# Optimization experiments

Measured on AMD Instinct MI355X. Metric: run time of the kernel, lower is better.

Reference implementation:

```python
import jax, jax.numpy as jnp
import numpy as np
import math

NUM_HEADS = 8
LN_EPS = 1e-8


def setup_inputs() -> dict:
    key = jax.random.key(0)
    ks = jax.random.split(key, 8)
    B, S, D = 16, 1024, 1024
    s = 1.0 / math.sqrt(D)
    return {
        "queries": jax.random.normal(ks[0], (B, S, D), dtype=jnp.float32),
        "keys": jax.random.normal(ks[1], (B, S, D), dtype=jnp.float32),
        "Wq": jax.random.normal(ks[2], (D, D), dtype=jnp.float32) * s,
        "bq": jnp.zeros((D,), dtype=jnp.float32),
        "Wk": jax.random.normal(ks[3], (D, D), dtype=jnp.float32) * s,
        "bk": jnp.zeros((D,), dtype=jnp.float32),
        "Wv": jax.random.normal(ks[4], (D, D), dtype=jnp.float32) * s,
        "bv": jnp.zeros((D,), dtype=jnp.float32),
        "ln_gamma": jnp.ones((D,), dtype=jnp.float32),
        "ln_beta": jnp.zeros((D,), dtype=jnp.float32),
    }


def _split_heads(x, H):
    # [B, S, D] -> [B*H, S, D/H], batch-major flattening (b*H + h), matching torch
    B, S, D = x.shape
    d = D // H
    return x.reshape(B, S, H, d).transpose(0, 2, 1, 3).reshape(B * H, S, d)


def _merge_heads(x, B, H):
    # [B*H, S, d] -> [B, S, H*d]
    BH, S, d = x.shape
    return x.reshape(B, H, S, d).transpose(0, 2, 1, 3).reshape(B, S, H * d)


def reference(queries, keys, Wq, bq, Wk, bk, Wv, bv, ln_gamma, ln_beta):
    B, S, D = queries.shape
    K_len = keys.shape[1]
    H = NUM_HEADS

    # ReLU'd QKV projections (nn.Linear uses x @ W.T + b)
    Q = jax.nn.relu(jnp.einsum("bsd,ed->bse", queries, Wq) + bq)
    K = jax.nn.relu(jnp.einsum("bsd,ed->bse", keys, Wk) + bk)
    V = jax.nn.relu(jnp.einsum("bsd,ed->bse", keys, Wv) + bv)

    Q_ = _split_heads(Q, H)  # [B*H, S, d]
    K_ = _split_heads(K, H)
    V_ = _split_heads(V, H)
    d_k = K_.shape[-1]

    scores = jnp.einsum("nsd,ntd->nst", Q_, K_) / jnp.sqrt(jnp.float32(d_k))
    attn = jax.nn.softmax(scores, axis=-1)  # [B*H, S, K_len]

    # post-softmax multiplicative mask: mask of nonzero query rows, tiled
    # head-major (mask.repeat(H,1,1)) exactly as the torch code does
    mask = (jnp.sum(jnp.abs(queries), axis=-1, keepdims=True) > 0).astype(queries.dtype)  # [B, S, 1]
    mask = jnp.broadcast_to(mask, (B, S, K_len))
    mask = jnp.tile(mask, (H, 1, 1))  # [H*B, S, K_len], index i -> batch i % B
    attn = attn * mask
    # dropout is identity in eval mode

    out = jnp.einsum("nst,ntd->nsd", attn, V_)  # [B*H, S, d]
    out = _merge_heads(out, B, H)  # [B, S, D]
    out = out + queries

    # LayerNorm over last dim, eps=1e-8
    mu = jnp.mean(out, axis=-1, keepdims=True)
    var = jnp.mean(jnp.square(out - mu), axis=-1, keepdims=True)
    out = (out - mu) / jnp.sqrt(var + LN_EPS) * ln_gamma + ln_beta
    return out
```

## Files before the change

kernel.cpp:

```cpp
#include <hip/hip_runtime.h>
#include <hip/hip_bf16.h>

#define B_ 16
#define S_ 1024
#define D_ 1024
#define H_ 8

typedef __attribute__((ext_vector_type(4))) float f32x4;
typedef __attribute__((ext_vector_type(8))) short s16x8;
typedef __attribute__((ext_vector_type(4))) short s16x4;
typedef unsigned int u32;

static __device__ __forceinline__ short f2bf(float x) {
  union { __hip_bfloat16 h; short s; } cv;
  cv.h = __float2bfloat16(x);
  return cv.s;
}
static __device__ __forceinline__ float bf2f(short x) {
  union { float f; u32 u; } cv;
  cv.u = ((u32)(unsigned short)x) << 16;
  return cv.f;
}
static __device__ __forceinline__ void async16(const void* g, void* l) {
  __builtin_amdgcn_global_load_lds((const __attribute__((address_space(1))) u32*)g,
                                   (__attribute__((address_space(3))) u32*)l, 16, 0, 0);
}

__global__ __launch_bounds__(256) void cvt_bf16(const float* __restrict__ s,
                                                short* __restrict__ d, int n8) {
  int i = blockIdx.x * 256 + threadIdx.x;
  if (i >= n8) return;
  const float4* s4 = (const float4*)s;
  float4 a = s4[2 * i], b = s4[2 * i + 1];
  s16x8 r;
  r[0] = f2bf(a.x); r[1] = f2bf(a.y); r[2] = f2bf(a.z); r[3] = f2bf(a.w);
  r[4] = f2bf(b.x); r[5] = f2bf(b.y); r[6] = f2bf(b.z); r[7] = f2bf(b.w);
  *(s16x8*)(d + (size_t)i * 8) = r;
}

__global__ __launch_bounds__(256, 2) void gemm_qkv(
    const short* __restrict__ qb, const short* __restrict__ kb,
    const short* __restrict__ wq, const short* __restrict__ wk,
    const short* __restrict__ wv, const float* __restrict__ bq,
    const float* __restrict__ bk, const float* __restrict__ bv,
    short* __restrict__ Qb, short* __restrict__ Kb, short* __restrict__ Vb) {
  __shared__ short lA[128 * 64];
  __shared__ short lB[128 * 64];
  const short* A; const short* W; const float* bias; short* C;
  switch (blockIdx.z) {
    case 0:  A = qb; W = wq; bias = bq; C = Qb; break;
    case 1:  A = kb; W = wk; bias = bk; C = Kb; break;
    default: A = kb; W = wv; bias = bv; C = Vb; break;
  }
  const int t = threadIdx.x;
  const int w = t >> 6, l = t & 63, lg = l >> 4, li = l & 15;
  const int wr = w >> 1, wc = w & 1;
  const int m0 = blockIdx.y << 7, n0 = blockIdx.x << 7;

  f32x4 acc[4][4];
#pragma unroll
  for (int m = 0; m < 4; ++m)
#pragma unroll
    for (int n = 0; n < 4; ++n) acc[m][n] = {0.f, 0.f, 0.f, 0.f};

  const char* Ab = (const char*)A + (size_t)m0 * 2048;
  const char* Wb = (const char*)W + (size_t)n0 * 2048;

#pragma unroll 1
  for (int k0 = 0; k0 < 1024; k0 += 64) {
    __syncthreads();
#pragma unroll
    for (int it = 0; it < 4; ++it) {
      int e = it * 256 + t;
      int row = e >> 3;
      int sb = ((e & 7) << 4) ^ ((row & 7) << 4);
      async16(Ab + (size_t)row * 2048 + k0 * 2 + sb, (char*)lA + e * 16);
      async16(Wb + (size_t)row * 2048 + k0 * 2 + sb, (char*)lB + e * 16);
    }
    __syncthreads();
#pragma unroll
    for (int kk = 0; kk < 2; ++kk) {
      s16x8 af[4], bfr[4];
#pragma unroll
      for (int m = 0; m < 4; ++m) {
        int row = wr * 64 + m * 16 + li;
        af[m] = *(const s16x8*)((char*)lA + row * 128 +
                                ((kk * 64 + (lg << 4)) ^ ((row & 7) << 4)));
      }
#pragma unroll
      for (int n = 0; n < 4; ++n) {
        int row = wc * 64 + n * 16 + li;
        bfr[n] = *(const s16x8*)((char*)lB + row * 128 +
                                 ((kk * 64 + (lg << 4)) ^ ((row & 7) << 4)));
      }
#pragma unroll
      for (int m = 0; m < 4; ++m)
#pragma unroll
        for (int n = 0; n < 4; ++n)
          acc[m][n] = __builtin_amdgcn_mfma_f32_16x16x32_bf16(af[m], bfr[n],
                                                              acc[m][n], 0, 0, 0);
    }
  }
#pragma unroll
  for (int n = 0; n < 4; ++n) {
    int col = n0 + wc * 64 + n * 16 + li;
    float bb = bias[col];
#pragma unroll
    for (int m = 0; m < 4; ++m) {
      int row0 = m0 + wr * 64 + m * 16 + (lg << 2);
#pragma unroll
      for (int r = 0; r < 4; ++r) {
        float v = acc[m][n][r] + bb;
        C[(size_t)(row0 + r) * 1024 + col] = f2bf(v > 0.f ? v : 0.f);
      }
    }
  }
}

__global__ __launch_bounds__(256, 2) void attn_kernel(
    const short* __restrict__ Qb, const short* __restrict__ Kb,
    const short* __restrict__ Vb, short* __restrict__ Ob) {
  __shared__ short lK[64 * 128];
  __shared__ short lV[128 * 72];
  __shared__ short lP[128 * 64];

  const int t = threadIdx.x;
  const int w = t >> 6, l = t & 63, lg = l >> 4, li = l & 15;
  const int bh = blockIdx.y;
  const int b = bh >> 3, h = bh & 7;
  const int q0 = blockIdx.x << 7;
  const size_t hbase = (size_t)b * (S_ * D_) + h * 128;

  s16x8 qf[2][4];
#pragma unroll
  for (int m = 0; m < 2; ++m)
#pragma unroll
    for (int kk = 0; kk < 4; ++kk) {
      int row = q0 + (w << 5) + m * 16 + li;
      qf[m][kk] = *(const s16x8*)(Qb + hbase + (size_t)row * D_ + kk * 32 + (lg << 3));
    }

  f32x4 o[2][8];
#pragma unroll
  for (int m = 0; m < 2; ++m)
#pragma unroll
    for (int nd = 0; nd < 8; ++nd) o[m][nd] = {0.f, 0.f, 0.f, 0.f};
  float mrow[2][4], lrow[2][4];
#pragma unroll
  for (int m = 0; m < 2; ++m)
#pragma unroll
    for (int r = 0; r < 4; ++r) { mrow[m][r] = -1e30f; lrow[m][r] = 0.f; }

  const float scale = 0.08838834764831845f;

#pragma unroll 1
  for (int kt = 0; kt < 16; ++kt) {
    __syncthreads();
    const char* Kt = (const char*)(Kb + hbase) + (size_t)(kt * 64) * 2048;
#pragma unroll
    for (int it = 0; it < 4; ++it) {
      int e = it * 256 + t;
      int krow = e >> 4;
      int sb = ((e & 15) << 4) ^ ((krow & 7) << 4);
      async16(Kt + (size_t)krow * 2048 + sb, (char*)lK + e * 16);
    }
    const short* Vt = Vb + hbase + (size_t)(kt * 64) * D_;
#pragma unroll
    for (int it = 0; it < 4; ++it) {
      int e = it * 256 + t;
      int vrow = e >> 4;
      int d0 = (e & 15) << 3;
      s16x8 vv = *(const s16x8*)(Vt + (size_t)vrow * D_ + d0);
      int kb2 = (vrow << 1) ^ ((e & 7) << 4);
      char* dst = (char*)lV + (size_t)d0 * 144 + kb2;
#pragma unroll
      for (int j = 0; j < 8; ++j) *(short*)(dst + j * 144) = vv[j];
    }
    __syncthreads();

    f32x4 sc[2][4];
#pragma unroll
    for (int m = 0; m < 2; ++m)
#pragma unroll
      for (int n = 0; n < 4; ++n) sc[m][n] = {0.f, 0.f, 0.f, 0.f};
#pragma unroll
    for (int kk = 0; kk < 4; ++kk)
#pragma unroll
      for (int n = 0; n < 4; ++n) {
        int krow = n * 16 + li;
        s16x8 kf = *(const s16x8*)((char*)lK + krow * 256 +
                                   ((kk * 64 + (lg << 4)) ^ ((krow & 7) << 4)));
        sc[0][n] = __builtin_amdgcn_mfma_f32_16x16x32_bf16(qf[0][kk], kf, sc[0][n], 0, 0, 0);
        sc[1][n] = __builtin_amdgcn_mfma_f32_16x16x32_bf16(qf[1][kk], kf, sc[1][n], 0, 0, 0);
      }

#pragma unroll
    for (int m = 0; m < 2; ++m)
#pragma unroll
      for (int r = 0; r < 4; ++r) {
        float v = fmaxf(fmaxf(sc[m][0][r], sc[m][1][r]), fmaxf(sc[m][2][r], sc[m][3][r]));
        v = fmaxf(v, __shfl_xor(v, 1));
        v = fmaxf(v, __shfl_xor(v, 2));
        v = fmaxf(v, __shfl_xor(v, 4));
        v = fmaxf(v, __shfl_xor(v, 8));
        float mnew = fmaxf(mrow[m][r], v);
        float f = __expf((mrow[m][r] - mnew) * scale);
        mrow[m][r] = mnew;
        float ps = 0.f;
#pragma unroll
        for (int n = 0; n < 4; ++n) {
          float p = __expf((sc[m][n][r] - mnew) * scale);
          sc[m][n][r] = p;
          ps += p;
        }
        ps += __shfl_xor(ps, 1);
        ps += __shfl_xor(ps, 2);
        ps += __shfl_xor(ps, 4);
        ps += __shfl_xor(ps, 8);
        lrow[m][r] = lrow[m][r] * f + ps;
#pragma unroll
        for (int nd = 0; nd < 8; ++nd) o[m][nd][r] *= f;
      }

#pragma unroll
    for (int m = 0; m < 2; ++m)
#pragma unroll
      for (int n = 0; n < 4; ++n)
#pragma unroll
        for (int r = 0; r < 4; ++r) {
          int prow = (w << 5) + m * 16 + (lg << 2) + r;
          int cb = ((n * 16 + li) << 1) ^ ((prow & 7) << 4);
          *(short*)((char*)lP + prow * 128 + cb) = f2bf(sc[m][n][r]);
        }
    asm volatile("s_waitcnt lgkmcnt(0)" ::: "memory");
    __builtin_amdgcn_sched_barrier(0);

#pragma unroll
    for (int ks = 0; ks < 2; ++ks) {
      int prow0 = (w << 5) + li;
      int prow1 = prow0 + 16;
      int kb3 = ks * 64 + (lg << 4);
      s16x8 pf0 = *(const s16x8*)((char*)lP + prow0 * 128 + (kb3 ^ ((prow0 & 7) << 4)));
      s16x8 pf1 = *(const s16x8*)((char*)lP + prow1 * 128 + (kb3 ^ ((prow1 & 7) << 4)));
#pragma unroll
      for (int nd = 0; nd < 8; ++nd) {
        int d = nd * 16 + li;
        s16x8 vf = *(const s16x8*)((char*)lV + d * 144 +
                                   (kb3 ^ (((d >> 3) & 7) << 4)));
        o[0][nd] = __builtin_amdgcn_mfma_f32_16x16x32_bf16(pf0, vf, o[0][nd], 0, 0, 0);
        o[1][nd] = __builtin_amdgcn_mfma_f32_16x16x32_bf16(pf1, vf, o[1][nd], 0, 0, 0);
      }
    }
  }

#pragma unroll
  for (int m = 0; m < 2; ++m)
#pragma unroll
    for (int r = 0; r < 4; ++r) {
      float inv = 1.f / lrow[m][r];
      int row = q0 + (w << 5) + m * 16 + (lg << 2) + r;
      short* orow = Ob + hbase + (size_t)row * D_;
#pragma unroll
      for (int nd = 0; nd < 8; ++nd)
        orow[nd * 16 + li] = f2bf(o[m][nd][r] * inv);
    }
}

__global__ __launch_bounds__(256) void ln_ep(const float* __restrict__ q,
                                             const short* __restrict__ Ob,
                                             const float* __restrict__ gam,
                                             const float* __restrict__ bet,
                                             float* __restrict__ out) {
  __shared__ float red[4][8];
  const int t = threadIdx.x;
  const int w = t >> 6, l = t & 63;
  const size_t off = (size_t)blockIdx.x * 1024 + t * 4;
  float4 qv = *(const float4*)(q + off);
  s16x4 ov = *(const s16x4*)(Ob + off);
  float oa[4] = {bf2f(ov[0]), bf2f(ov[1]), bf2f(ov[2]), bf2f(ov[3])};
  float qa[4] = {qv.x, qv.y, qv.z, qv.w};
  float s0 = 0, s1 = 0, s2 = 0, s3 = 0, s4 = 0, s5 = 0;
#pragma unroll
  for (int j = 0; j < 4; ++j) {
    s0 += fabsf(qa[j]);
    s1 += oa[j];
    s2 += qa[j];
    s3 += oa[j] * oa[j];
    s4 += oa[j] * qa[j];
    s5 += qa[j] * qa[j];
  }
#pragma unroll
  for (int d2 = 1; d2 < 64; d2 <<= 1) {
    s0 += __shfl_xor(s0, d2); s1 += __shfl_xor(s1, d2); s2 += __shfl_xor(s2, d2);
    s3 += __shfl_xor(s3, d2); s4 += __shfl_xor(s4, d2); s5 += __shfl_xor(s5, d2);
  }
  if (l == 0) {
    red[w][0] = s0; red[w][1] = s1; red[w][2] = s2;
    red[w][3] = s3; red[w][4] = s4; red[w][5] = s5;
  }
  __syncthreads();
  s0 = red[0][0] + red[1][0] + red[2][0] + red[3][0];
  s1 = red[0][1] + red[1][1] + red[2][1] + red[3][1];
  s2 = red[0][2] + red[1][2] + red[2][2] + red[3][2];
  s3 = red[0][3] + red[1][3] + red[2][3] + red[3][3];
  s4 = red[0][4] + red[1][4] + red[2][4] + red[3][4];
  s5 = red[0][5] + red[1][5] + red[2][5] + red[3][5];
  float msk = s0 > 0.f ? 1.f : 0.f;
  float sy = msk * s1 + s2;
  float sy2 = msk * s3 + 2.f * msk * s4 + s5;
  float mean = sy * (1.f / 1024.f);
  float var = sy2 * (1.f / 1024.f) - mean * mean;
  float inv = rsqrtf(fmaxf(var, 0.f) + 1e-8f);
  float4 gv = *(const float4*)(gam + t * 4);
  float4 bv = *(const float4*)(bet + t * 4);
  float4 rr;
  rr.x = (msk * oa[0] + qa[0] - mean) * inv * gv.x + bv.x;
  rr.y = (msk * oa[1] + qa[1] - mean) * inv * gv.y + bv.y;
  rr.z = (msk * oa[2] + qa[2] - mean) * inv * gv.z + bv.z;
  rr.w = (msk * oa[3] + qa[3] - mean) * inv * gv.w + bv.w;
  *(float4*)(out + off) = rr;
}

extern "C" void kernel_launch(void* const* d_in, const int* in_sizes, int n_in,
                              void* d_out, int out_size, void* d_ws, size_t ws_size,
                              hipStream_t stream) {
  const float* q   = (const float*)d_in[0];
  const float* k   = (const float*)d_in[1];
  const float* Wq  = (const float*)d_in[2];
  const float* bq  = (const float*)d_in[3];
  const float* Wk  = (const float*)d_in[4];
  const float* bk  = (const float*)d_in[5];
  const float* Wv  = (const float*)d_in[6];
  const float* bv  = (const float*)d_in[7];
  const float* gam = (const float*)d_in[8];
  const float* bet = (const float*)d_in[9];
  float* out = (float*)d_out;

  short* qb  = (short*)d_ws;
  short* kb  = qb + 16777216;
  short* wqb = kb + 16777216;
  short* wkb = wqb + 1048576;
  short* wvb = wkb + 1048576;
  short* Qb  = wvb + 1048576;
  short* Kb  = Qb + 16777216;
  short* Vb  = Kb + 16777216;
  short* Ob  = qb;

  cvt_bf16<<<8192, 256, 0, stream>>>(q, qb, 2097152);
  cvt_bf16<<<8192, 256, 0, stream>>>(k, kb, 2097152);
  cvt_bf16<<<512, 256, 0, stream>>>(Wq, wqb, 131072);
  cvt_bf16<<<512, 256, 0, stream>>>(Wk, wkb, 131072);
  cvt_bf16<<<512, 256, 0, stream>>>(Wv, wvb, 131072);
  gemm_qkv<<<dim3(8, 128, 3), 256, 0, stream>>>(qb, kb, wqb, wkb, wvb,
                                                bq, bk, bv, Qb, Kb, Vb);
  attn_kernel<<<dim3(8, 128), 256, 0, stream>>>(Qb, Kb, Vb, Ob);
  ln_ep<<<16384, 256, 0, stream>>>(q, Ob, gam, bet, out);
}
```

Measured before the change: 510.7 us.

## Prefetch K/V tiles in registers, fold softmax scale into Q, lazy rescale

The attention kernel now prefetches the next K/V tile into registers while computing the current one, replacing async global-to-LDS copies. V is stored transposed with packed pair writes and a padded layout. The softmax scale and log2(e) are folded into Q in the QKV GEMM epilogue so softmax can use hardware exp2. The running-max rescale is skipped when the new max stays within a threshold. The change also remaps attention workgroup indices and merges the five conversion launches into two. It costs extra registers, and the lazy rescale and the bf16 rounding of the pre-scaled Q shift numerics slightly.

Result: faster. 486.2 us (-4.8%).

```diff
diff --git a/kernel.cpp b/kernel.cpp
--- a/kernel.cpp
+++ b/kernel.cpp
@@ -21,21 +21,55 @@
   cv.u = ((u32)(unsigned short)x) << 16;
   return cv.f;
 }
+static __device__ __forceinline__ float exp2_hw(float x) {
+  float r;
+  asm("v_exp_f32 %0, %1" : "=v"(r) : "v"(x));
+  return r;
+}
 static __device__ __forceinline__ void async16(const void* g, void* l) {
   __builtin_amdgcn_global_load_lds((const __attribute__((address_space(1))) u32*)g,
                                    (__attribute__((address_space(3))) u32*)l, 16, 0, 0);
 }
 
-__global__ __launch_bounds__(256) void cvt_bf16(const float* __restrict__ s,
-                                                short* __restrict__ d, int n8) {
+#define QSCALE 0.12751741530f
+
+__global__ __launch_bounds__(256) void cvt_qk(const float* __restrict__ q,
+                                              const float* __restrict__ k,
+                                              short* __restrict__ qb,
+                                              short* __restrict__ kb) {
   int i = blockIdx.x * 256 + threadIdx.x;
-  if (i >= n8) return;
+  const float* s;
+  short* d;
+  int j;
+  if (i < 2097152) { s = q; d = qb; j = i; }
+  else             { s = k; d = kb; j = i - 2097152; }
   const float4* s4 = (const float4*)s;
-  float4 a = s4[2 * i], b = s4[2 * i + 1];
+  float4 a = s4[2 * j], b = s4[2 * j + 1];
   s16x8 r;
   r[0] = f2bf(a.x); r[1] = f2bf(a.y); r[2] = f2bf(a.z); r[3] = f2bf(a.w);
   r[4] = f2bf(b.x); r[5] = f2bf(b.y); r[6] = f2bf(b.z); r[7] = f2bf(b.w);
-  *(s16x8*)(d + (size_t)i * 8) = r;
+  *(s16x8*)(d + (size_t)j * 8) = r;
+}
+
+__global__ __launch_bounds__(256) void cvt_w(const float* __restrict__ wq,
+                                             const float* __restrict__ wk,
+                                             const float* __restrict__ wv,
+                                             short* __restrict__ dq,
+                                             short* __restrict__ dk,
+                                             short* __restrict__ dv) {
+  int i = blockIdx.x * 256 + threadIdx.x;
+  const float* s;
+  short* d;
+  int j;
+  if (i < 131072)      { s = wq; d = dq; j = i; }
+  else if (i < 262144) { s = wk; d = dk; j = i - 131072; }
+  else                 { s = wv; d = dv; j = i - 262144; }
+  const float4* s4 = (const float4*)s;
+  float4 a = s4[2 * j], b = s4[2 * j + 1];
+  s16x8 r;
+  r[0] = f2bf(a.x); r[1] = f2bf(a.y); r[2] = f2bf(a.z); r[3] = f2bf(a.w);
+  r[4] = f2bf(b.x); r[5] = f2bf(b.y); r[6] = f2bf(b.z); r[7] = f2bf(b.w);
+  *(s16x8*)(d + (size_t)j * 8) = r;
 }
 
 __global__ __launch_bounds__(256, 2) void gemm_qkv(
@@ -47,10 +81,11 @@
   __shared__ short lA[128 * 64];
   __shared__ short lB[128 * 64];
   const short* A; const short* W; const float* bias; short* C;
+  float scl;
   switch (blockIdx.z) {
-    case 0:  A = qb; W = wq; bias = bq; C = Qb; break;
-    case 1:  A = kb; W = wk; bias = bk; C = Kb; break;
-    default: A = kb; W = wv; bias = bv; C = Vb; break;
+    case 0:  A = qb; W = wq; bias = bq; C = Qb; scl = QSCALE; break;
+    case 1:  A = kb; W = wk; bias = bk; C = Kb; scl = 1.f; break;
+    default: A = kb; W = wv; bias = bv; C = Vb; scl = 1.f; break;
   }
   const int t = threadIdx.x;
   const int w = t >> 6, l = t & 63, lg = l >> 4, li = l & 15;
@@ -111,7 +146,8 @@
 #pragma unroll
       for (int r = 0; r < 4; ++r) {
         float v = acc[m][n][r] + bb;
-        C[(size_t)(row0 + r) * 1024 + col] = f2bf(v > 0.f ? v : 0.f);
+        v = (v > 0.f ? v : 0.f) * scl;
+        C[(size_t)(row0 + r) * 1024 + col] = f2bf(v);
       }
     }
   }
@@ -121,15 +157,18 @@
     const short* __restrict__ Qb, const short* __restrict__ Kb,
     const short* __restrict__ Vb, short* __restrict__ Ob) {
   __shared__ short lK[64 * 128];
-  __shared__ short lV[128 * 72];
+  __shared__ short lV[128 * 88];
   __shared__ short lP[128 * 64];
 
   const int t = threadIdx.x;
   const int w = t >> 6, l = t & 63, lg = l >> 4, li = l & 15;
-  const int bh = blockIdx.y;
+  const int wgid = blockIdx.x;
+  const int bh = ((wgid & 7) << 4) + (wgid >> 6);
+  const int q0 = ((wgid >> 3) & 7) << 7;
   const int b = bh >> 3, h = bh & 7;
-  const int q0 = blockIdx.x << 7;
   const size_t hbase = (size_t)b * (S_ * D_) + h * 128;
+  const short* Kh = Kb + hbase;
+  const short* Vh = Vb + hbase;
 
   s16x8 qf[2][4];
 #pragma unroll
@@ -151,32 +190,46 @@
 #pragma unroll
     for (int r = 0; r < 4; ++r) { mrow[m][r] = -1e30f; lrow[m][r] = 0.f; }
 
-  const float scale = 0.08838834764831845f;
+  s16x8 kreg[4], vr0[2], vr1[2];
+#define LOADT(KT)                                                              \
+  {                                                                            \
+    _Pragma("unroll") for (int it = 0; it < 4; ++it) {                         \
+      int e = it * 256 + t;                                                    \
+      kreg[it] = *(const s16x8*)(Kh + (size_t)((KT)*64 + (e >> 4)) * 1024 +    \
+                                 (e & 15) * 8);                                \
+    }                                                                          \
+    _Pragma("unroll") for (int vit = 0; vit < 2; ++vit) {                      \
+      int e2 = vit * 256 + t;                                                  \
+      int k0 = (e2 & 31) * 2, d0 = (e2 >> 5) * 8;                              \
+      vr0[vit] = *(const s16x8*)(Vh + (size_t)((KT)*64 + k0) * 1024 + d0);     \
+      vr1[vit] = *(const s16x8*)(Vh + (size_t)((KT)*64 + k0 + 1) * 1024 + d0); \
+    }                                                                          \
+  }
+
+  LOADT(0);
 
 #pragma unroll 1
   for (int kt = 0; kt < 16; ++kt) {
     __syncthreads();
-    const char* Kt = (const char*)(Kb + hbase) + (size_t)(kt * 64) * 2048;
 #pragma unroll
     for (int it = 0; it < 4; ++it) {
       int e = it * 256 + t;
-      int krow = e >> 4;
-      int sb = ((e & 15) << 4) ^ ((krow & 7) << 4);
-      async16(Kt + (size_t)krow * 2048 + sb, (char*)lK + e * 16);
-    }
-    const short* Vt = Vb + hbase + (size_t)(kt * 64) * D_;
-#pragma unroll
-    for (int it = 0; it < 4; ++it) {
-      int e = it * 256 + t;
-      int vrow = e >> 4;
-      int d0 = (e & 15) << 3;
-      s16x8 vv = *(const s16x8*)(Vt + (size_t)vrow * D_ + d0);
-      int kb2 = (vrow << 1) ^ ((e & 7) << 4);
-      char* dst = (char*)lV + (size_t)d0 * 144 + kb2;
-#pragma unroll
-      for (int j = 0; j < 8; ++j) *(short*)(dst + j * 144) = vv[j];
+      int kr = e >> 4, kc = e & 15;
+      *(s16x8*)((char*)lK + kr * 256 + ((kc * 16) ^ ((kr & 7) << 4))) = kreg[it];
+    }
+#pragma unroll
+    for (int vit = 0; vit < 2; ++vit) {
+      int e2 = vit * 256 + t;
+      int k0 = (e2 & 31) * 2, d0 = (e2 >> 5) * 8;
+#pragma unroll
+      for (int j = 0; j < 8; ++j) {
+        u32 pk = (u32)(unsigned short)vr0[vit][j] |
+                 ((u32)(unsigned short)vr1[vit][j] << 16);
+        *(u32*)((char*)lV + (d0 + j) * 176 + k0 * 2) = pk;
+      }
     }
     __syncthreads();
+    if (kt < 15) LOADT(kt + 1);
 
     f32x4 sc[2][4];
 #pragma unroll
@@ -194,22 +247,42 @@
         sc[1][n] = __builtin_amdgcn_mfma_f32_16x16x32_bf16(qf[1][kk], kf, sc[1][n], 0, 0, 0);
       }
 
+    float tm[2][4];
+    bool skip = true;
 #pragma unroll
     for (int m = 0; m < 2; ++m)
 #pragma unroll
       for (int r = 0; r < 4; ++r) {
-        float v = fmaxf(fmaxf(sc[m][0][r], sc[m][1][r]), fmaxf(sc[m][2][r], sc[m][3][r]));
+        float v = fmaxf(fmaxf(sc[m][0][r], sc[m][1][r]),
+                        fmaxf(sc[m][2][r], sc[m][3][r]));
         v = fmaxf(v, __shfl_xor(v, 1));
         v = fmaxf(v, __shfl_xor(v, 2));
         v = fmaxf(v, __shfl_xor(v, 4));
         v = fmaxf(v, __shfl_xor(v, 8));
-        float mnew = fmaxf(mrow[m][r], v);
-        float f = __expf((mrow[m][r] - mnew) * scale);
-        mrow[m][r] = mnew;
+        tm[m][r] = v;
+        skip = skip && (v <= mrow[m][r] + 11.5f);
+      }
+    if (!__all(skip)) {
+#pragma unroll
+      for (int m = 0; m < 2; ++m)
+#pragma unroll
+        for (int r = 0; r < 4; ++r) {
+          float mnew = fmaxf(mrow[m][r], tm[m][r]);
+          float fsc = exp2_hw(mrow[m][r] - mnew);
+          mrow[m][r] = mnew;
+          lrow[m][r] *= fsc;
+#pragma unroll
+          for (int nd = 0; nd < 8; ++nd) o[m][nd][r] *= fsc;
+        }
+    }
+#pragma unroll
+    for (int m = 0; m < 2; ++m)
+#pragma unroll
+      for (int r = 0; r < 4; ++r) {
         float ps = 0.f;
 #pragma unroll
         for (int n = 0; n < 4; ++n) {
-          float p = __expf((sc[m][n][r] - mnew) * scale);
+          float p = exp2_hw(sc[m][n][r] - mrow[m][r]);
           sc[m][n][r] = p;
           ps += p;
         }
@@ -217,9 +290,7 @@
         ps += __shfl_xor(ps, 2);
         ps += __shfl_xor(ps, 4);
         ps += __shfl_xor(ps, 8);
-        lrow[m][r] = lrow[m][r] * f + ps;
-#pragma unroll
-        for (int nd = 0; nd < 8; ++nd) o[m][nd][r] *= f;
+        lrow[m][r] += ps;
       }
 
 #pragma unroll
@@ -245,13 +316,13 @@
 #pragma unroll
       for (int nd = 0; nd < 8; ++nd) {
         int d = nd * 16 + li;
-        s16x8 vf = *(const s16x8*)((char*)lV + d * 144 +
-                                   (kb3 ^ (((d >> 3) & 7) << 4)));
+        s16x8 vf = *(const s16x8*)((char*)lV + d * 176 + kb3);
         o[0][nd] = __builtin_amdgcn_mfma_f32_16x16x32_bf16(pf0, vf, o[0][nd], 0, 0, 0);
         o[1][nd] = __builtin_amdgcn_mfma_f32_16x16x32_bf16(pf1, vf, o[1][nd], 0, 0, 0);
       }
     }
   }
+#undef LOADT
 
 #pragma unroll
   for (int m = 0; m < 2; ++m)
@@ -346,13 +417,10 @@
   short* Vb  = Kb + 16777216;
   short* Ob  = qb;
 
-  cvt_bf16<<<8192, 256, 0, stream>>>(q, qb, 2097152);
-  cvt_bf16<<<8192, 256, 0, stream>>>(k, kb, 2097152);
-  cvt_bf16<<<512, 256, 0, stream>>>(Wq, wqb, 131072);
-  cvt_bf16<<<512, 256, 0, stream>>>(Wk, wkb, 131072);
-  cvt_bf16<<<512, 256, 0, stream>>>(Wv, wvb, 131072);
+  cvt_qk<<<16384, 256, 0, stream>>>(q, k, qb, kb);
+  cvt_w<<<1536, 256, 0, stream>>>(Wq, Wk, Wv, wqb, wkb, wvb);
   gemm_qkv<<<dim3(8, 128, 3), 256, 0, stream>>>(qb, kb, wqb, wkb, wvb,
                                                 bq, bk, bv, Qb, Kb, Vb);
-  attn_kernel<<<dim3(8, 128), 256, 0, stream>>>(Qb, Kb, Vb, Ob);
+  attn_kernel<<<1024, 256, 0, stream>>>(Qb, Kb, Vb, Ob);
   ln_ep<<<16384, 256, 0, stream>>>(q, Ob, gam, bet, out);
 }
```
